# Kernel optimization log

Hardware: AMD Instinct MI355X
Metric: run time of the kernel (lower is better)

## Reference

```python
import jax, jax.numpy as jnp
import numpy as np
import math

D_MODEL = 1024
NUM_HEADS = 16


def setup_inputs() -> dict:
    key = jax.random.key(0)
    ks = jax.random.split(key, 5)
    B, S, D = 4, 2048, D_MODEL
    scale = 1.0 / math.sqrt(D)
    x = jax.random.normal(ks[0], (B, S, D), dtype=jnp.float32)
    wq = jax.random.normal(ks[1], (D, D), dtype=jnp.float32) * scale
    wk = jax.random.normal(ks[2], (D, D), dtype=jnp.float32) * scale
    wv = jax.random.normal(ks[3], (D, D), dtype=jnp.float32) * scale
    wo = jax.random.normal(ks[4], (D, D), dtype=jnp.float32) * scale
    return {"x": x, "wq": wq, "wk": wk, "wv": wv, "wo": wo}


def _mhsa(x, wq, wk, wv, wo):
    B, S, D = x.shape
    H = NUM_HEADS
    dk = D // H
    # projections: y = x @ W^T
    q = (x @ wq.T).reshape(B, S, H, dk).transpose(0, 2, 1, 3)  # [B,H,S,dk]
    k = (x @ wk.T).reshape(B, S, H, dk).transpose(0, 2, 1, 3)
    v = (x @ wv.T).reshape(B, S, H, dk).transpose(0, 2, 1, 3)
    scores = jnp.einsum("bhqd,bhkd->bhqk", q, k) / jnp.sqrt(jnp.asarray(dk, x.dtype))
    mask = jnp.tril(jnp.ones((S, S), dtype=bool))  # [S,S] causal
    neg_inf = jnp.asarray(-jnp.inf, scores.dtype)
    scores_masked = jnp.where(mask, scores, neg_inf)
    max_scores = jnp.max(scores_masked, axis=-1, keepdims=True)
    max_scores = jnp.where(jnp.isfinite(max_scores), max_scores, jnp.zeros_like(max_scores))
    exp_scores = jnp.exp(scores - max_scores) * mask.astype(scores.dtype)
    denom = jnp.maximum(exp_scores.sum(axis=-1, keepdims=True), 1e-9)
    attn = exp_scores / denom
    out = jnp.einsum("bhqk,bhkd->bhqd", attn, v)  # [B,H,S,dk]
    out = out.transpose(0, 2, 1, 3).reshape(B, S, D)
    return out @ wo.T


def reference(x, wq, wk, wv, wo):
    return _mhsa(x, wq, wk, wv, wo)
```

## Files before the change

kernel.cpp:

```cpp
#include <hip/hip_runtime.h>
#include <stdint.h>


typedef __attribute__((ext_vector_type(8))) short short8;
typedef __attribute__((ext_vector_type(4))) short short4v;
typedef __attribute__((ext_vector_type(4))) float float4v;

#define EXP_C1 0.18033688011112042f
#define EXP_C2 5.770780163555852f

__device__ inline short f2bf(float f) {
  union { float f; uint32_t u; } v; v.f = f;
  uint32_t r = (v.u + 0x7fffu + ((v.u >> 16) & 1)) >> 16;
  return (short)(uint16_t)r;
}

__device__ inline void async_copy16(const void* g, void* l) {
  __builtin_amdgcn_global_load_lds(
      (const __attribute__((address_space(1))) void*)g,
      (__attribute__((address_space(3))) void*)l, 16, 0, 0);
}

__global__ __launch_bounds__(256) void cvt(const float* __restrict__ s,
                                           short* __restrict__ d, int n4) {
  const int i = blockIdx.x * 256 + threadIdx.x;
  if (i < n4) {
    const float4v v = *(const float4v*)(s + 4 * (size_t)i);
    short4v o;
    o[0] = f2bf(v[0]); o[1] = f2bf(v[1]);
    o[2] = f2bf(v[2]); o[3] = f2bf(v[3]);
    *(short4v*)(d + 4 * (size_t)i) = o;
  }
}

__global__ __launch_bounds__(256) void cvtW(
    const float* __restrict__ a, const float* __restrict__ b,
    const float* __restrict__ c, const float* __restrict__ e,
    short* __restrict__ oa, short* __restrict__ ob,
    short* __restrict__ oc, short* __restrict__ oe) {
  const float* s = (blockIdx.y == 0) ? a : (blockIdx.y == 1) ? b
                   : (blockIdx.y == 2) ? c : e;
  short* d = (blockIdx.y == 0) ? oa : (blockIdx.y == 1) ? ob
             : (blockIdx.y == 2) ? oc : oe;
  const int i = blockIdx.x * 256 + threadIdx.x;
  const float4v v = *(const float4v*)(s + 4 * (size_t)i);
  short4v o;
  o[0] = f2bf(v[0]); o[1] = f2bf(v[1]);
  o[2] = f2bf(v[2]); o[3] = f2bf(v[3]);
  *(short4v*)(d + 4 * (size_t)i) = o;
}

template <int MODE>
__global__ __launch_bounds__(256) void gemm_bt(
    const short* __restrict__ A,
    const short* __restrict__ W0, const short* __restrict__ W1,
    const short* __restrict__ W2,
    short* __restrict__ Yb0, short* __restrict__ Yb1, short* __restrict__ Yb2,
    float* __restrict__ Yf) {
  constexpr int Kd = 1024;
  __shared__ __align__(16) short As[128 * 32];
  __shared__ __align__(16) short Bs[128 * 32];

  const int t = threadIdx.x;
  const int w = t >> 6, l = t & 63, l15 = l & 15, quad = l >> 4;
  const int wm = w >> 1, wn = w & 1;
  const int m0 = blockIdx.y * 128, n0 = blockIdx.x * 128;

  const short* W = W0;
  short* Yb = Yb0;
  if (MODE == 0) {
    if (blockIdx.z == 1) { W = W1; Yb = Yb1; }
    else if (blockIdx.z == 2) { W = W2; Yb = Yb2; }
  }

  float4v acc[4][4];
#pragma unroll
  for (int i = 0; i < 4; i++)
#pragma unroll
    for (int j = 0; j < 4; j++) acc[i][j] = (float4v){0.f, 0.f, 0.f, 0.f};

  const int r4 = t >> 2, c48 = (t & 3) * 8;
  const short* Wbase = W + (n0 + r4) * Kd + c48;
  short* AsW = &As[w * 512];
  short* BsW = &Bs[w * 512];
  const int i0 = m0 + r4;
  const int i1 = m0 + 64 + r4;

  for (int k0 = 0; k0 < Kd; k0 += 32) {
    if (MODE == 0) {
      async_copy16(A + (size_t)i0 * Kd + k0 + c48, AsW);
      async_copy16(A + (size_t)i1 * Kd + k0 + c48, AsW + 2048);
    } else {
      const int k = k0 + c48, h = k >> 6, dd = k & 63;
      async_copy16(A + ((((size_t)(i0 >> 11) * 16 + h) * 2048 + (i0 & 2047)) * 64 + dd), AsW);
      async_copy16(A + ((((size_t)(i1 >> 11) * 16 + h) * 2048 + (i1 & 2047)) * 64 + dd), AsW + 2048);
    }
    async_copy16(Wbase + k0, BsW);
    async_copy16(Wbase + 64 * Kd + k0, BsW + 2048);
    __syncthreads();
    short8 af[4], bf[4];
#pragma unroll
    for (int mi = 0; mi < 4; mi++)
      af[mi] = *(const short8*)&As[(wm * 64 + mi * 16 + l15) * 32 + quad * 8];
#pragma unroll
    for (int ni = 0; ni < 4; ni++)
      bf[ni] = *(const short8*)&Bs[(wn * 64 + ni * 16 + l15) * 32 + quad * 8];
#pragma unroll
    for (int mi = 0; mi < 4; mi++)
#pragma unroll
      for (int ni = 0; ni < 4; ni++)
        acc[mi][ni] = __builtin_amdgcn_mfma_f32_16x16x32_bf16(
            af[mi], bf[ni], acc[mi][ni], 0, 0, 0);
    __syncthreads();
  }

#pragma unroll
  for (int mi = 0; mi < 4; mi++) {
    const int ib = m0 + wm * 64 + mi * 16 + quad * 4;
#pragma unroll
    for (int ni = 0; ni < 4; ni++) {
      const int j = n0 + wn * 64 + ni * 16 + l15;
#pragma unroll
      for (int r = 0; r < 4; r++) {
        const int i = ib + r;
        if (MODE == 0) {
          Yb[((((size_t)(i >> 11) * 16 + (j >> 6)) * 2048 + (i & 2047)) * 64 + (j & 63))] =
              f2bf(acc[mi][ni][r]);
        } else {
          Yf[(size_t)i * 1024 + j] = acc[mi][ni][r];
        }
      }
    }
  }
}

__global__ __launch_bounds__(256) void transV(const short* __restrict__ V,
                                              short* __restrict__ VT) {
  __shared__ __align__(16) short Ls[64 * 72];
  const int t = threadIdx.x;
  const int s0 = blockIdx.x * 64, bh = blockIdx.y;
  const short* Vh = V + (size_t)bh * 2048 * 64;
  short* Th = VT + (size_t)bh * 64 * 2048;
  const int r = t >> 2, c = (t & 3) * 16;
  *(short8*)&Ls[r * 72 + c] = *(const short8*)&Vh[(size_t)(s0 + r) * 64 + c];
  *(short8*)&Ls[r * 72 + c + 8] = *(const short8*)&Vh[(size_t)(s0 + r) * 64 + c + 8];
  __syncthreads();
  short8 o0, o1;
#pragma unroll
  for (int j = 0; j < 8; j++) {
    o0[j] = Ls[(c + j) * 72 + r];
    o1[j] = Ls[(c + 8 + j) * 72 + r];
  }
  *(short8*)&Th[(size_t)r * 2048 + s0 + c] = o0;
  *(short8*)&Th[(size_t)r * 2048 + s0 + c + 8] = o1;
}

__global__ __launch_bounds__(256) void attn3(
    short* __restrict__ Q,
    const short* __restrict__ K,
    const short* __restrict__ VT) {
  __shared__ __align__(16) short Ks[64 * 72];
  __shared__ __align__(16) short Vs[64 * 72];
  __shared__ __align__(16) short Ps[4 * 16 * 72];

  const int t = threadIdx.x;
  const int w = t >> 6, l = t & 63, l15 = l & 15, quad = l >> 4;
  const int bh = blockIdx.y;
  short* Qh = Q + (size_t)bh * 2048 * 64;
  const short* Kh = K + (size_t)bh * 2048 * 64;
  const short* Vh = VT + (size_t)bh * 64 * 2048;
  const int sr = t >> 2, scc = (t & 3) * 16;
  short* PsW = &Ps[w * 16 * 72];

  short8 ones;
#pragma unroll
  for (int j = 0; j < 8; j++) ones[j] = (short)0x3F80;

  for (int pass = 0; pass < 2; pass++) {
    const int q0 = (pass ? (31 - blockIdx.x) : blockIdx.x) * 64;
    const int qn = q0 + w * 16 + l15;
    const short8 qf0 = *(const short8*)&Qh[(size_t)qn * 64 + quad * 8];
    const short8 qf1 = *(const short8*)&Qh[(size_t)qn * 64 + 32 + quad * 8];

    float4v acc[4];
#pragma unroll
    for (int dt = 0; dt < 4; dt++) acc[dt] = (float4v){0.f, 0.f, 0.f, 0.f};
    float4v accL = (float4v){0.f, 0.f, 0.f, 0.f};

    short8 kv0 = *(const short8*)&Kh[(size_t)sr * 64 + scc];
    short8 kv1 = *(const short8*)&Kh[(size_t)sr * 64 + scc + 8];
    short8 vv0 = *(const short8*)&Vh[(size_t)sr * 2048 + scc];
    short8 vv1 = *(const short8*)&Vh[(size_t)sr * 2048 + scc + 8];

    for (int kb = 0; kb <= q0; kb += 64) {
      const bool diag = (kb == q0);
      *(short8*)&Ks[sr * 72 + scc] = kv0;
      *(short8*)&Ks[sr * 72 + scc + 8] = kv1;
      *(short8*)&Vs[sr * 72 + scc] = vv0;
      *(short8*)&Vs[sr * 72 + scc + 8] = vv1;
      __syncthreads();

      const int kb2 = diag ? kb : kb + 64;
      kv0 = *(const short8*)&Kh[(size_t)(kb2 + sr) * 64 + scc];
      kv1 = *(const short8*)&Kh[(size_t)(kb2 + sr) * 64 + scc + 8];
      vv0 = *(const short8*)&Vh[(size_t)sr * 2048 + kb2 + scc];
      vv1 = *(const short8*)&Vh[(size_t)sr * 2048 + kb2 + scc + 8];

#pragma unroll
      for (int kt = 0; kt < 4; kt++) {
        const short8 kf0 = *(const short8*)&Ks[(kt * 16 + l15) * 72 + quad * 8];
        const short8 kf1 = *(const short8*)&Ks[(kt * 16 + l15) * 72 + 32 + quad * 8];
        float4v s = (float4v){0.f, 0.f, 0.f, 0.f};
        s = __builtin_amdgcn_mfma_f32_16x16x32_bf16(kf0, qf0, s, 0, 0, 0);
        s = __builtin_amdgcn_mfma_f32_16x16x32_bf16(kf1, qf1, s, 0, 0, 0);
        short4v pw;
        if (diag) {
#pragma unroll
          for (int ri = 0; ri < 4; ri++) {
            const int key = kb + kt * 16 + quad * 4 + ri;
            const float p = __builtin_amdgcn_exp2f(s[ri] * EXP_C1 - EXP_C2);
            pw[ri] = f2bf((key <= qn) ? p : 0.f);
          }
        } else {
#pragma unroll
          for (int ri = 0; ri < 4; ri++)
            pw[ri] = f2bf(__builtin_amdgcn_exp2f(s[ri] * EXP_C1 - EXP_C2));
        }
        *(short4v*)&PsW[l15 * 72 + kt * 16 + quad * 4] = pw;
      }
      __builtin_amdgcn_wave_barrier();

      const short8 pf0 = *(const short8*)&PsW[l15 * 72 + quad * 8];
      const short8 pf1 = *(const short8*)&PsW[l15 * 72 + 32 + quad * 8];
#pragma unroll
      for (int dt = 0; dt < 4; dt++) {
        const short8 vf0 = *(const short8*)&Vs[(dt * 16 + l15) * 72 + quad * 8];
        const short8 vf1 = *(const short8*)&Vs[(dt * 16 + l15) * 72 + 32 + quad * 8];
        acc[dt] = __builtin_amdgcn_mfma_f32_16x16x32_bf16(vf0, pf0, acc[dt], 0, 0, 0);
        acc[dt] = __builtin_amdgcn_mfma_f32_16x16x32_bf16(vf1, pf1, acc[dt], 0, 0, 0);
      }
      accL = __builtin_amdgcn_mfma_f32_16x16x32_bf16(ones, pf0, accL, 0, 0, 0);
      accL = __builtin_amdgcn_mfma_f32_16x16x32_bf16(ones, pf1, accL, 0, 0, 0);
      __syncthreads();
    }

    const float inv = 1.0f / fmaxf(accL[0], 1e-30f);
#pragma unroll
    for (int dt = 0; dt < 4; dt++) {
      short4v o;
#pragma unroll
      for (int ri = 0; ri < 4; ri++) o[ri] = f2bf(acc[dt][ri] * inv);
      *(short4v*)&Qh[(size_t)qn * 64 + dt * 16 + quad * 4] = o;
    }
  }
}

extern "C" void kernel_launch(void* const* d_in, const int* in_sizes, int n_in,
                              void* d_out, int out_size, void* d_ws,
                              size_t ws_size, hipStream_t stream) {
  const float* x = (const float*)d_in[0];
  const float* wq = (const float*)d_in[1];
  const float* wk = (const float*)d_in[2];
  const float* wv = (const float*)d_in[3];
  const float* wo = (const float*)d_in[4];
  float* out = (float*)d_out;

  short* xb = (short*)d_out;
  short* vtg = xb + (size_t)8192 * 1024;

  short* wqb = (short*)d_ws;
  short* wkb = wqb + (size_t)1024 * 1024;
  short* wvb = wkb + (size_t)1024 * 1024;
  short* wob = wvb + (size_t)1024 * 1024;
  short* qws = wob + (size_t)1024 * 1024;
  short* kws = qws + (size_t)8192 * 1024;
  short* vws = kws + (size_t)8192 * 1024;

  cvt<<<8192, 256, 0, stream>>>(x, xb, 2097152);
  cvtW<<<dim3(1024, 4), 256, 0, stream>>>(wq, wk, wv, wo, wqb, wkb, wvb, wob);

  gemm_bt<0><<<dim3(8, 64, 3), 256, 0, stream>>>(
      xb, wqb, wkb, wvb, qws, kws, vws, nullptr);
  transV<<<dim3(32, 64), 256, 0, stream>>>(vws, vtg);
  attn3<<<dim3(16, 64), 256, 0, stream>>>(qws, kws, vtg);
  gemm_bt<1><<<dim3(8, 64, 1), 256, 0, stream>>>(
      qws, wob, nullptr, nullptr, nullptr, nullptr, nullptr, out);
}
```

Baseline: 282.0 us.

## Double-buffer attention K/V tiles, swizzle LDS, fold softmax scale into Q projection

The attention kernel now double-buffers K and V tiles in shared memory, which removes the trailing barrier in each key-block iteration. It also replaces padded LDS rows with an XOR swizzle, folds the softmax scale into the Q projection epilogue, and seeds the score MFMA with the exp offset. Probabilities are packed to bf16 by truncation using a byte permute instead of round-to-nearest, which slightly changes numerics. The two conversion kernels are merged into one launch. LDS use rises because of the double buffers.

```diff
diff --git a/kernel.cpp b/kernel.cpp
--- a/kernel.cpp
+++ b/kernel.cpp
@@ -5,8 +5,9 @@
 typedef __attribute__((ext_vector_type(8))) short short8;
 typedef __attribute__((ext_vector_type(4))) short short4v;
 typedef __attribute__((ext_vector_type(4))) float float4v;
-
-#define EXP_C1 0.18033688011112042f
+typedef __attribute__((ext_vector_type(2))) unsigned int uint2v;
+
+#define QSCALE 0.18033688011112042f
 #define EXP_C2 5.770780163555852f
 
 __device__ inline short f2bf(float f) {
@@ -15,39 +16,38 @@
   return (short)(uint16_t)r;
 }
 
+__device__ inline unsigned int pack2bf(float a, float b) {
+  union { float f; unsigned int u; } ua, ub;
+  ua.f = a; ub.f = b;
+  return __builtin_amdgcn_perm(ub.u, ua.u, 0x07060302u);
+}
+
 __device__ inline void async_copy16(const void* g, void* l) {
   __builtin_amdgcn_global_load_lds(
       (const __attribute__((address_space(1))) void*)g,
       (__attribute__((address_space(3))) void*)l, 16, 0, 0);
 }
 
-__global__ __launch_bounds__(256) void cvt(const float* __restrict__ s,
-                                           short* __restrict__ d, int n4) {
-  const int i = blockIdx.x * 256 + threadIdx.x;
-  if (i < n4) {
-    const float4v v = *(const float4v*)(s + 4 * (size_t)i);
-    short4v o;
-    o[0] = f2bf(v[0]); o[1] = f2bf(v[1]);
-    o[2] = f2bf(v[2]); o[3] = f2bf(v[3]);
-    *(short4v*)(d + 4 * (size_t)i) = o;
-  }
-}
-
-__global__ __launch_bounds__(256) void cvtW(
-    const float* __restrict__ a, const float* __restrict__ b,
-    const float* __restrict__ c, const float* __restrict__ e,
-    short* __restrict__ oa, short* __restrict__ ob,
-    short* __restrict__ oc, short* __restrict__ oe) {
-  const float* s = (blockIdx.y == 0) ? a : (blockIdx.y == 1) ? b
-                   : (blockIdx.y == 2) ? c : e;
-  short* d = (blockIdx.y == 0) ? oa : (blockIdx.y == 1) ? ob
-             : (blockIdx.y == 2) ? oc : oe;
-  const int i = blockIdx.x * 256 + threadIdx.x;
-  const float4v v = *(const float4v*)(s + 4 * (size_t)i);
+__global__ __launch_bounds__(256) void cvtAll(
+    const float* __restrict__ x, const float* __restrict__ wq,
+    const float* __restrict__ wk, const float* __restrict__ wv,
+    const float* __restrict__ wo,
+    short* __restrict__ xb, short* __restrict__ wqb, short* __restrict__ wkb,
+    short* __restrict__ wvb, short* __restrict__ wob) {
+  const int b = blockIdx.x;
+  const float* s; short* d; int base;
+  if (b < 8192) { s = x; d = xb; base = b; }
+  else {
+    const int wi = (b - 8192) >> 10; base = (b - 8192) & 1023;
+    s = (wi == 0) ? wq : (wi == 1) ? wk : (wi == 2) ? wv : wo;
+    d = (wi == 0) ? wqb : (wi == 1) ? wkb : (wi == 2) ? wvb : wob;
+  }
+  const size_t i = (size_t)base * 256 + threadIdx.x;
+  const float4v v = *(const float4v*)(s + 4 * i);
   short4v o;
   o[0] = f2bf(v[0]); o[1] = f2bf(v[1]);
   o[2] = f2bf(v[2]); o[3] = f2bf(v[3]);
-  *(short4v*)(d + 4 * (size_t)i) = o;
+  *(short4v*)(d + 4 * i) = o;
 }
 
 template <int MODE>
@@ -68,9 +68,11 @@
 
   const short* W = W0;
   short* Yb = Yb0;
+  float sc = 1.0f;
   if (MODE == 0) {
-    if (blockIdx.z == 1) { W = W1; Yb = Yb1; }
-    else if (blockIdx.z == 2) { W = W2; Yb = Yb2; }
+    if (blockIdx.z == 0) sc = QSCALE;
+    else if (blockIdx.z == 1) { W = W1; Yb = Yb1; }
+    else { W = W2; Yb = Yb2; }
   }
 
   float4v acc[4][4];
@@ -125,7 +127,7 @@
         const int i = ib + r;
         if (MODE == 0) {
           Yb[((((size_t)(i >> 11) * 16 + (j >> 6)) * 2048 + (i & 2047)) * 64 + (j & 63))] =
-              f2bf(acc[mi][ni][r]);
+              f2bf(acc[mi][ni][r] * sc);
         } else {
           Yf[(size_t)i * 1024 + j] = acc[mi][ni][r];
         }
@@ -155,13 +157,13 @@
   *(short8*)&Th[(size_t)r * 2048 + s0 + c + 8] = o1;
 }
 
-__global__ __launch_bounds__(256) void attn3(
+__global__ __launch_bounds__(256) void attn4(
     short* __restrict__ Q,
     const short* __restrict__ K,
     const short* __restrict__ VT) {
-  __shared__ __align__(16) short Ks[64 * 72];
-  __shared__ __align__(16) short Vs[64 * 72];
-  __shared__ __align__(16) short Ps[4 * 16 * 72];
+  __shared__ __align__(16) short Ks[2][64 * 64];
+  __shared__ __align__(16) short Vs[2][64 * 64];
+  __shared__ __align__(16) short Ps[4][16 * 64];
 
   const int t = threadIdx.x;
   const int w = t >> 6, l = t & 63, l15 = l & 15, quad = l >> 4;
@@ -169,12 +171,23 @@
   short* Qh = Q + (size_t)bh * 2048 * 64;
   const short* Kh = K + (size_t)bh * 2048 * 64;
   const short* Vh = VT + (size_t)bh * 64 * 2048;
-  const int sr = t >> 2, scc = (t & 3) * 16;
-  short* PsW = &Ps[w * 16 * 72];
+
+  const int sr = t >> 2, c0 = t & 3;
+  const int ssw = sr & 7;
+  const int stA = sr * 64 + (((2 * c0) ^ ssw) << 3);
+  const int stB = sr * 64 + (((2 * c0 + 1) ^ ssw) << 3);
+  const int gA = c0 * 16, gB = c0 * 16 + 8;
+
+  const int fsw = l15 & 7;
+  const int fc0 = (quad ^ fsw) << 3;
+  const int fc1 = ((4 + quad) ^ fsw) << 3;
+  short* PsW = &Ps[w][0];
+  const int pwr = l15 * 64;
 
   short8 ones;
 #pragma unroll
   for (int j = 0; j < 8; j++) ones[j] = (short)0x3F80;
+  const float4v initC = (float4v){-EXP_C2, -EXP_C2, -EXP_C2, -EXP_C2};
 
   for (int pass = 0; pass < 2; pass++) {
     const int q0 = (pass ? (31 - blockIdx.x) : blockIdx.x) * 64;
@@ -187,61 +200,66 @@
     for (int dt = 0; dt < 4; dt++) acc[dt] = (float4v){0.f, 0.f, 0.f, 0.f};
     float4v accL = (float4v){0.f, 0.f, 0.f, 0.f};
 
-    short8 kv0 = *(const short8*)&Kh[(size_t)sr * 64 + scc];
-    short8 kv1 = *(const short8*)&Kh[(size_t)sr * 64 + scc + 8];
-    short8 vv0 = *(const short8*)&Vh[(size_t)sr * 2048 + scc];
-    short8 vv1 = *(const short8*)&Vh[(size_t)sr * 2048 + scc + 8];
-
-    for (int kb = 0; kb <= q0; kb += 64) {
+    short8 kv0 = *(const short8*)&Kh[(size_t)sr * 64 + gA];
+    short8 kv1 = *(const short8*)&Kh[(size_t)sr * 64 + gB];
+    short8 vv0 = *(const short8*)&Vh[(size_t)sr * 2048 + gA];
+    short8 vv1 = *(const short8*)&Vh[(size_t)sr * 2048 + gB];
+
+    int p = 0;
+    for (int kb = 0; kb <= q0; kb += 64, p ^= 1) {
       const bool diag = (kb == q0);
-      *(short8*)&Ks[sr * 72 + scc] = kv0;
-      *(short8*)&Ks[sr * 72 + scc + 8] = kv1;
-      *(short8*)&Vs[sr * 72 + scc] = vv0;
-      *(short8*)&Vs[sr * 72 + scc + 8] = vv1;
+      short* KsP = &Ks[p][0];
+      short* VsP = &Vs[p][0];
+      *(short8*)&KsP[stA] = kv0;
+      *(short8*)&KsP[stB] = kv1;
+      *(short8*)&VsP[stA] = vv0;
+      *(short8*)&VsP[stB] = vv1;
       __syncthreads();
 
       const int kb2 = diag ? kb : kb + 64;
-      kv0 = *(const short8*)&Kh[(size_t)(kb2 + sr) * 64 + scc];
-      kv1 = *(const short8*)&Kh[(size_t)(kb2 + sr) * 64 + scc + 8];
-      vv0 = *(const short8*)&Vh[(size_t)sr * 2048 + kb2 + scc];
-      vv1 = *(const short8*)&Vh[(size_t)sr * 2048 + kb2 + scc + 8];
+      kv0 = *(const short8*)&Kh[(size_t)(kb2 + sr) * 64 + gA];
+      kv1 = *(const short8*)&Kh[(size_t)(kb2 + sr) * 64 + gB];
+      vv0 = *(const short8*)&Vh[(size_t)sr * 2048 + kb2 + gA];
+      vv1 = *(const short8*)&Vh[(size_t)sr * 2048 + kb2 + gB];
 
 #pragma unroll
       for (int kt = 0; kt < 4; kt++) {
-        const short8 kf0 = *(const short8*)&Ks[(kt * 16 + l15) * 72 + quad * 8];
-        const short8 kf1 = *(const short8*)&Ks[(kt * 16 + l15) * 72 + 32 + quad * 8];
-        float4v s = (float4v){0.f, 0.f, 0.f, 0.f};
-        s = __builtin_amdgcn_mfma_f32_16x16x32_bf16(kf0, qf0, s, 0, 0, 0);
+        const int krb = (kt * 16 + l15) * 64;
+        const short8 kf0 = *(const short8*)&KsP[krb + fc0];
+        const short8 kf1 = *(const short8*)&KsP[krb + fc1];
+        float4v s = __builtin_amdgcn_mfma_f32_16x16x32_bf16(kf0, qf0, initC, 0, 0, 0);
         s = __builtin_amdgcn_mfma_f32_16x16x32_bf16(kf1, qf1, s, 0, 0, 0);
-        short4v pw;
+        float p0 = __builtin_amdgcn_exp2f(s[0]);
+        float p1 = __builtin_amdgcn_exp2f(s[1]);
+        float p2 = __builtin_amdgcn_exp2f(s[2]);
+        float p3 = __builtin_amdgcn_exp2f(s[3]);
         if (diag) {
-#pragma unroll
-          for (int ri = 0; ri < 4; ri++) {
-            const int key = kb + kt * 16 + quad * 4 + ri;
-            const float p = __builtin_amdgcn_exp2f(s[ri] * EXP_C1 - EXP_C2);
-            pw[ri] = f2bf((key <= qn) ? p : 0.f);
-          }
-        } else {
-#pragma unroll
-          for (int ri = 0; ri < 4; ri++)
-            pw[ri] = f2bf(__builtin_amdgcn_exp2f(s[ri] * EXP_C1 - EXP_C2));
+          const int key = kb + kt * 16 + quad * 4;
+          p0 = (key <= qn) ? p0 : 0.f;
+          p1 = (key + 1 <= qn) ? p1 : 0.f;
+          p2 = (key + 2 <= qn) ? p2 : 0.f;
+          p3 = (key + 3 <= qn) ? p3 : 0.f;
         }
-        *(short4v*)&PsW[l15 * 72 + kt * 16 + quad * 4] = pw;
+        uint2v pw;
+        pw[0] = pack2bf(p0, p1);
+        pw[1] = pack2bf(p2, p3);
+        *(uint2v*)&PsW[pwr + (((2 * kt + (quad >> 1)) ^ fsw) << 3) +
+                       ((quad & 1) << 2)] = pw;
       }
       __builtin_amdgcn_wave_barrier();
 
-      const short8 pf0 = *(const short8*)&PsW[l15 * 72 + quad * 8];
-      const short8 pf1 = *(const short8*)&PsW[l15 * 72 + 32 + quad * 8];
+      const short8 pf0 = *(const short8*)&PsW[pwr + fc0];
+      const short8 pf1 = *(const short8*)&PsW[pwr + fc1];
 #pragma unroll
       for (int dt = 0; dt < 4; dt++) {
-        const short8 vf0 = *(const short8*)&Vs[(dt * 16 + l15) * 72 + quad * 8];
-        const short8 vf1 = *(const short8*)&Vs[(dt * 16 + l15) * 72 + 32 + quad * 8];
+        const int vrb = (dt * 16 + l15) * 64;
+        const short8 vf0 = *(const short8*)&VsP[vrb + fc0];
+        const short8 vf1 = *(const short8*)&VsP[vrb + fc1];
         acc[dt] = __builtin_amdgcn_mfma_f32_16x16x32_bf16(vf0, pf0, acc[dt], 0, 0, 0);
         acc[dt] = __builtin_amdgcn_mfma_f32_16x16x32_bf16(vf1, pf1, acc[dt], 0, 0, 0);
       }
       accL = __builtin_amdgcn_mfma_f32_16x16x32_bf16(ones, pf0, accL, 0, 0, 0);
       accL = __builtin_amdgcn_mfma_f32_16x16x32_bf16(ones, pf1, accL, 0, 0, 0);
-      __syncthreads();
     }
 
     const float inv = 1.0f / fmaxf(accL[0], 1e-30f);
@@ -252,6 +270,7 @@
       for (int ri = 0; ri < 4; ri++) o[ri] = f2bf(acc[dt][ri] * inv);
       *(short4v*)&Qh[(size_t)qn * 64 + dt * 16 + quad * 4] = o;
     }
+    if (pass == 0) __syncthreads();
   }
 }
 
@@ -276,13 +295,11 @@
   short* kws = qws + (size_t)8192 * 1024;
   short* vws = kws + (size_t)8192 * 1024;
 
-  cvt<<<8192, 256, 0, stream>>>(x, xb, 2097152);
-  cvtW<<<dim3(1024, 4), 256, 0, stream>>>(wq, wk, wv, wo, wqb, wkb, wvb, wob);
-
+  cvtAll<<<12288, 256, 0, stream>>>(x, wq, wk, wv, wo, xb, wqb, wkb, wvb, wob);
   gemm_bt<0><<<dim3(8, 64, 3), 256, 0, stream>>>(
       xb, wqb, wkb, wvb, qws, kws, vws, nullptr);
   transV<<<dim3(32, 64), 256, 0, stream>>>(vws, vtg);
-  attn3<<<dim3(16, 64), 256, 0, stream>>>(qws, kws, vtg);
+  attn4<<<dim3(16, 64), 256, 0, stream>>>(qws, kws, vtg);
   gemm_bt<1><<<dim3(8, 64, 1), 256, 0, stream>>>(
       qws, wob, nullptr, nullptr, nullptr, nullptr, nullptr, out);
 }
```

After: 284.3 us. About the same (+0.8%).
